# Performance work log

Hardware: AMD Instinct MI355X
Metric: run time of the kernel (lower is better)

Reference implementation:

```python
import jax, jax.numpy as jnp
import numpy as np
from math import sqrt


def setup_inputs() -> dict:
    key = jax.random.key(0)
    k1, k2, k3, k4, k5 = jax.random.split(key, 5)
    B, L, H, D = 16, 4096, 16, 64
    S, M = 4096, 256
    queries = jax.random.normal(k1, (B, L, H, D), dtype=jnp.float32)
    keys = jax.random.normal(k2, (B, S, H, D), dtype=jnp.float32)
    values = jax.random.normal(k3, (B, S, H, D), dtype=jnp.float32)
    # nn.Linear(L_k=S, M): weight [M, S], bias [M]
    squeeze_w = jax.random.normal(k4, (M, S), dtype=jnp.float32) / sqrt(S)
    squeeze_b = jax.random.normal(k5, (M,), dtype=jnp.float32) * 0.01
    return {"queries": queries, "keys": keys, "values": values,
            "squeeze_w": squeeze_w, "squeeze_b": squeeze_b}


def reference(queries, keys, values, squeeze_w, squeeze_b):
    # queries: [B,L,H,D]; keys/values: [B,S,H,D]; squeeze_w: [M,S]; squeeze_b: [M]
    B, L, H, D = queries.shape
    scale = 1.0 / sqrt(D)
    bias = squeeze_b[None, :, None, None]  # broadcast over [B,M,H,D]
    # Linear over the sequence axis S -> M (Linformer compression)
    keys_sq = jnp.einsum('bshd,ms->bmhd', keys, squeeze_w) + bias      # [B,M,H,D]
    values_sq = jnp.einsum('bshd,ms->bmhd', values, squeeze_w) + bias  # [B,M,H,D]
    # Scaled dot-product attention against compressed K/V
    attn = jnp.einsum('blhd,bmhd->bhlm', queries, keys_sq) * scale     # [B,H,L,M]
    attn = jax.nn.softmax(attn, axis=-1)  # dropout is identity in eval / p=0
    context = jnp.einsum('bhlm,bmhd->blhd', attn, values_sq)           # [B,L,H,D]
    return context
```

## Files before the change

kernel.cpp:

```cpp
#include <hip/hip_runtime.h>

#define NB 16
#define NL 4096
#define NH 16
#define ND 64
#define NS 4096
#define NM 256

typedef __fp16 f16;
typedef __attribute__((ext_vector_type(8)))  __fp16 f16x8;
typedef __attribute__((ext_vector_type(4)))  __fp16 f16x4;
typedef __attribute__((ext_vector_type(2)))  __fp16 f16x2;
typedef __attribute__((ext_vector_type(4)))  float  f32x4;
typedef __attribute__((ext_vector_type(16))) float  f32x16;

__device__ __forceinline__ void gload_lds16(const void* g, void* l) {
  __builtin_amdgcn_global_load_lds(
      (const __attribute__((address_space(1))) void*)g,
      (__attribute__((address_space(3))) void*)l, 16, 0, 0);
}

__device__ __forceinline__ int pk2(float a, float b) {
  f16x2 t = __builtin_amdgcn_cvt_pkrtz(a, b);
  union { f16x2 h; int i; } u; u.h = t; return u.i;
}

__global__ __launch_bounds__(256) void k_wcvt(const float* __restrict__ W,
                                              f16* __restrict__ W16) {
  const int i = blockIdx.x * 256 + threadIdx.x;
  f32x4 v = ((const f32x4*)W)[i];
  f16x2 a = __builtin_amdgcn_cvt_pkrtz(v[0], v[1]);
  f16x2 b = __builtin_amdgcn_cvt_pkrtz(v[2], v[3]);
  f16x4 o; o[0] = a[0]; o[1] = a[1]; o[2] = b[0]; o[3] = b[1];
  ((f16x4*)W16)[i] = o;
}

__global__ __launch_bounds__(256, 2) void k_squeeze(
    const f16* __restrict__ W16, const float* __restrict__ keys,
    const float* __restrict__ values, const float* __restrict__ bias,
    f16* __restrict__ Ksq, f16* __restrict__ Vsq) {
  const int h = blockIdx.x & 15;
  const int b = (blockIdx.x >> 4) & 15;
  const int t = blockIdx.x >> 8;
  const float* __restrict__ X = t ? values : keys;

  __shared__ __align__(16) f16 Wt[256 * 64];
  __shared__ __align__(16) f16 XT[64 * 72];

  const int tid  = threadIdx.x;
  const int lane = tid & 63;
  const int w    = tid >> 6;
  const int l31  = lane & 31;
  const int g    = lane >> 5;

  const int  wrsub = lane >> 3;
  const int  wslot = lane & 7;
  const char* Wg = (const char*)W16 + (long)wrsub * (NS * 2) + ((wslot * 16) ^ (wrsub << 4));

  const int sp  = tid & 31;
  const int ng0 = tid >> 5;
  const float* Xb = X + ((long)b * NS) * (NH * ND) + h * ND;

  f32x16 acc[2][2];
#pragma unroll
  for (int mi = 0; mi < 2; ++mi)
#pragma unroll
    for (int di = 0; di < 2; ++di)
#pragma unroll
      for (int q = 0; q < 16; ++q) acc[mi][di][q] = 0.f;

  f32x4 xr[2][2];
#pragma unroll
  for (int u = 0; u < 2; ++u)
#pragma unroll
    for (int r = 0; r < 2; ++r)
      xr[u][r] = *(const f32x4*)(Xb + (long)(2 * sp + r) * (NH * ND) + (ng0 + 8 * u) * 4);

  for (int kt = 0; kt < NS / 64; ++kt) {
    const int k0 = kt * 64;
    __syncthreads();
    {
      const char* wg = Wg + (long)k0 * 2;
#pragma unroll
      for (int i = 0; i < 8; ++i) {
        const int ii = w * 8 + i;
        gload_lds16(wg + (long)ii * 8 * (NS * 2), (char*)Wt + ii * 1024);
      }
    }
#pragma unroll
    for (int u = 0; u < 2; ++u) {
      const int ng = ng0 + 8 * u;
#pragma unroll
      for (int c = 0; c < 4; ++c) {
        f16x2 p = __builtin_amdgcn_cvt_pkrtz(xr[u][0][c], xr[u][1][c]);
        *(f16x2*)((char*)XT + (ng * 4 + c) * 144 + sp * 4) = p;
      }
    }
    __syncthreads();
    if (kt + 1 < NS / 64) {
#pragma unroll
      for (int u = 0; u < 2; ++u)
#pragma unroll
        for (int r = 0; r < 2; ++r)
          xr[u][r] = *(const f32x4*)(Xb + (long)(k0 + 64 + 2 * sp + r) * (NH * ND) +
                                     (ng0 + 8 * u) * 4);
    }
#pragma unroll
    for (int ks = 0; ks < 4; ++ks) {
      f16x8 af[2], bf[2];
#pragma unroll
      for (int mi = 0; mi < 2; ++mi) {
        const int row  = w * 64 + mi * 32 + l31;
        const int colb = (ks * 32 + g * 16) ^ ((row & 7) << 4);
        af[mi] = *(const f16x8*)((const char*)Wt + row * 128 + colb);
      }
#pragma unroll
      for (int di = 0; di < 2; ++di) {
        const int n = di * 32 + l31;
        bf[di] = *(const f16x8*)((const char*)XT + n * 144 + ks * 32 + g * 16);
      }
#pragma unroll
      for (int mi = 0; mi < 2; ++mi)
#pragma unroll
        for (int di = 0; di < 2; ++di)
          acc[mi][di] =
              __builtin_amdgcn_mfma_f32_32x32x16_f16(af[mi], bf[di], acc[mi][di], 0, 0, 0);
    }
  }

  const long bh = b * 16 + h;
  if (t == 0) {
    f16* K = Ksq + bh * (NM * ND);
#pragma unroll
    for (int mi = 0; mi < 2; ++mi)
#pragma unroll
      for (int di = 0; di < 2; ++di)
#pragma unroll
        for (int r = 0; r < 16; ++r) {
          const int m = w * 64 + mi * 32 + (r & 3) + 8 * (r >> 2) + 4 * g;
          const int d = di * 32 + l31;
          K[((d >> 3) * 256 + m) * 8 + (d & 7)] = (f16)(acc[mi][di][r] + bias[m]);
        }
  } else {
    f16* V = Vsq + bh * (ND * NM);
#pragma unroll
    for (int mi = 0; mi < 2; ++mi)
#pragma unroll
      for (int di = 0; di < 2; ++di)
#pragma unroll
        for (int q = 0; q < 4; ++q) {
          const int m0 = w * 64 + mi * 32 + 8 * q + 4 * g;
          const int d  = di * 32 + l31;
          f16x2 p0 = __builtin_amdgcn_cvt_pkrtz(acc[mi][di][q * 4 + 0] + bias[m0 + 0],
                                                acc[mi][di][q * 4 + 1] + bias[m0 + 1]);
          f16x2 p1 = __builtin_amdgcn_cvt_pkrtz(acc[mi][di][q * 4 + 2] + bias[m0 + 2],
                                                acc[mi][di][q * 4 + 3] + bias[m0 + 3]);
          f16x4 pv; pv[0] = p0[0]; pv[1] = p0[1]; pv[2] = p1[0]; pv[3] = p1[1];
          *(f16x4*)(V + ((m0 >> 3) * 64 + d) * 8 + 4 * g) = pv;
        }
  }
}

__global__ __launch_bounds__(256, 2) void k_attn(const float* __restrict__ Q,
                                                 const f16* __restrict__ Ksq,
                                                 const f16* __restrict__ Vsq,
                                                 float* __restrict__ Out) {
  const int xcd   = blockIdx.x & 7;
  const int local = blockIdx.x >> 3;
  const int bh    = xcd * 32 + (local >> 1);
  const int chunk = local & 1;
  const int b = bh >> 4, h = bh & 15;

  __shared__ __align__(16) f16 Klds[8 * 256 * 8];
  __shared__ __align__(16) f16 Vlds[32 * 64 * 8];

  const int tid = threadIdx.x, lane = tid & 63, w = tid >> 6;
  const int q = lane & 31, hi = lane >> 5;

  const float* Qlane = Q   + (((long)b * NL + q) * NH + h) * ND;
  float*       Olane = Out + (((long)b * NL + q) * NH + h) * ND;
  const float  c = 0.125f * 1.44269504088896f;

  f32x4 qv[8];
  {
    const float* qp = Qlane + (long)(chunk * 2048 + w * 32) * (NH * ND) + hi * 8;
#pragma unroll
    for (int kt = 0; kt < 4; ++kt) {
      qv[2 * kt]     = *(const f32x4*)(qp + kt * 16);
      qv[2 * kt + 1] = *(const f32x4*)(qp + kt * 16 + 4);
    }
  }

  {
    const f16* Kg = Ksq + (long)bh * 16384;
    const f16* Vg = Vsq + (long)bh * 16384;
#pragma unroll
    for (int i = 0; i < 8; ++i)
      gload_lds16(Kg + w * 4096 + i * 512 + lane * 8, (char*)Klds + w * 8192 + i * 1024);
#pragma unroll
    for (int i = 0; i < 8; ++i)
      gload_lds16(Vg + w * 4096 + i * 512 + lane * 8, (char*)Vlds + w * 8192 + i * 1024);
  }
  __syncthreads();

  for (int it = 0; it < 16; ++it) {
    const int row0 = chunk * 2048 + it * 128 + w * 32;

    union { f16x8 v; f16x2 h2[4]; } qb[4];
#pragma unroll
    for (int kt = 0; kt < 4; ++kt) {
      qb[kt].h2[0] = __builtin_amdgcn_cvt_pkrtz(qv[2 * kt][0], qv[2 * kt][1]);
      qb[kt].h2[1] = __builtin_amdgcn_cvt_pkrtz(qv[2 * kt][2], qv[2 * kt][3]);
      qb[kt].h2[2] = __builtin_amdgcn_cvt_pkrtz(qv[2 * kt + 1][0], qv[2 * kt + 1][1]);
      qb[kt].h2[3] = __builtin_amdgcn_cvt_pkrtz(qv[2 * kt + 1][2], qv[2 * kt + 1][3]);
    }

    if (it + 1 < 16) {
      const float* qp = Qlane + (long)(row0 + 128) * (NH * ND) + hi * 8;
#pragma unroll
      for (int kt = 0; kt < 4; ++kt) {
        qv[2 * kt]     = *(const f32x4*)(qp + kt * 16);
        qv[2 * kt + 1] = *(const f32x4*)(qp + kt * 16 + 4);
      }
    }

    f32x16 sa[8];
#pragma unroll
    for (int mf = 0; mf < 8; ++mf)
#pragma unroll
      for (int r = 0; r < 16; ++r) sa[mf][r] = 0.f;

#pragma unroll
    for (int kt = 0; kt < 4; ++kt) {
#pragma unroll
      for (int mf = 0; mf < 8; ++mf) {
        f16x8 ka = *(const f16x8*)((const char*)Klds +
                                   ((2 * kt + hi) * 256 + mf * 32 + q) * 16);
        sa[mf] = __builtin_amdgcn_mfma_f32_32x32x16_f16(ka, qb[kt].v, sa[mf], 0, 0, 0);
      }
    }

    f32x16 mm = sa[0];
#pragma unroll
    for (int mf = 1; mf < 8; ++mf)
#pragma unroll
      for (int r = 0; r < 16; ++r) mm[r] = fmaxf(mm[r], sa[mf][r]);
    float m8_0 = fmaxf(mm[0], mm[8]),  m8_1 = fmaxf(mm[1], mm[9]);
    float m8_2 = fmaxf(mm[2], mm[10]), m8_3 = fmaxf(mm[3], mm[11]);
    float m8_4 = fmaxf(mm[4], mm[12]), m8_5 = fmaxf(mm[5], mm[13]);
    float m8_6 = fmaxf(mm[6], mm[14]), m8_7 = fmaxf(mm[7], mm[15]);
    float mx = fmaxf(fmaxf(fmaxf(m8_0, m8_1), fmaxf(m8_2, m8_3)),
                     fmaxf(fmaxf(m8_4, m8_5), fmaxf(m8_6, m8_7)));
    mx = fmaxf(mx, __shfl_xor(mx, 32));

#pragma unroll
    for (int mf = 0; mf < 8; ++mf)
#pragma unroll
      for (int r = 0; r < 16; ++r)
        sa[mf][r] = __builtin_amdgcn_exp2f((sa[mf][r] - mx) * c);

    f32x16 t0 = sa[0] + sa[1];
    f32x16 t1 = sa[2] + sa[3];
    f32x16 t2 = sa[4] + sa[5];
    f32x16 t3 = sa[6] + sa[7];
    t0 = (t0 + t1) + (t2 + t3);
    float s8_0 = t0[0] + t0[8],  s8_1 = t0[1] + t0[9];
    float s8_2 = t0[2] + t0[10], s8_3 = t0[3] + t0[11];
    float s8_4 = t0[4] + t0[12], s8_5 = t0[5] + t0[13];
    float s8_6 = t0[6] + t0[14], s8_7 = t0[7] + t0[15];
    float sum = ((s8_0 + s8_1) + (s8_2 + s8_3)) + ((s8_4 + s8_5) + (s8_6 + s8_7));
    sum += __shfl_xor(sum, 32);
    const float inv = 1.0f / sum;

    f32x16 o[2];
#pragma unroll
    for (int df = 0; df < 2; ++df)
#pragma unroll
      for (int r = 0; r < 16; ++r) o[df][r] = 0.f;

#pragma unroll
    for (int t = 0; t < 16; ++t) {
      const int fp = t >> 1, s = t & 1;
      int a0 = pk2(sa[fp][8 * s + 0] * inv, sa[fp][8 * s + 1] * inv);
      int a1 = pk2(sa[fp][8 * s + 2] * inv, sa[fp][8 * s + 3] * inv);
      int b0 = pk2(sa[fp][8 * s + 4] * inv, sa[fp][8 * s + 5] * inv);
      int b1 = pk2(sa[fp][8 * s + 6] * inv, sa[fp][8 * s + 7] * inv);
      asm volatile("v_permlane32_swap_b32 %0, %1" : "+v"(a0), "+v"(b0));
      asm volatile("v_permlane32_swap_b32 %0, %1" : "+v"(a1), "+v"(b1));
      union { int w4[4]; f16x8 v; } pb;
      pb.w4[0] = a0; pb.w4[1] = a1; pb.w4[2] = b0; pb.w4[3] = b1;
#pragma unroll
      for (int df = 0; df < 2; ++df) {
        f16x8 va = *(const f16x8*)((const char*)Vlds +
                                   ((2 * t + hi) * 64 + df * 32 + q) * 16);
        o[df] = __builtin_amdgcn_mfma_f32_32x32x16_f16(va, pb.v, o[df], 0, 0, 0);
      }
    }

    float* op = Olane + (long)row0 * (NH * ND);
#pragma unroll
    for (int df = 0; df < 2; ++df)
#pragma unroll
      for (int rq = 0; rq < 4; ++rq) {
        f32x4 st;
        st[0] = o[df][rq * 4 + 0]; st[1] = o[df][rq * 4 + 1];
        st[2] = o[df][rq * 4 + 2]; st[3] = o[df][rq * 4 + 3];
        *(f32x4*)(op + df * 32 + rq * 8 + hi * 4) = st;
      }
  }
}

extern "C" void kernel_launch(void* const* d_in, const int* in_sizes, int n_in,
                              void* d_out, int out_size, void* d_ws, size_t ws_size,
                              hipStream_t stream) {
  const float* Qp   = (const float*)d_in[0];
  const float* Kp   = (const float*)d_in[1];
  const float* Vp   = (const float*)d_in[2];
  const float* Wp   = (const float*)d_in[3];
  const float* bp   = (const float*)d_in[4];
  float*       Outp = (float*)d_out;

  char* ws = (char*)d_ws;
  f16* W16 = (f16*)ws;
  f16* Ksq = (f16*)(ws + (2l << 20));
  f16* Vsq = (f16*)(ws + (2l << 20) + (8l << 20));

  hipLaunchKernelGGL(k_wcvt, dim3(1024), dim3(256), 0, stream, Wp, W16);
  hipLaunchKernelGGL(k_squeeze, dim3(512), dim3(256), 0, stream, W16, Kp, Vp, bp, Ksq, Vsq);
  hipLaunchKernelGGL(k_attn, dim3(512), dim3(256), 0, stream, Qp, Ksq, Vsq, Outp);
}
```

Baseline: 315.0 us.

## Pre-swizzle squeeze weights into MFMA layout and read them directly from global

```diff
diff --git a/kernel.cpp b/kernel.cpp
--- a/kernel.cpp
+++ b/kernel.cpp
@@ -26,17 +26,23 @@
 }
 
 __global__ __launch_bounds__(256) void k_wcvt(const float* __restrict__ W,
-                                              f16* __restrict__ W16) {
-  const int i = blockIdx.x * 256 + threadIdx.x;
-  f32x4 v = ((const f32x4*)W)[i];
-  f16x2 a = __builtin_amdgcn_cvt_pkrtz(v[0], v[1]);
-  f16x2 b = __builtin_amdgcn_cvt_pkrtz(v[2], v[3]);
-  f16x4 o; o[0] = a[0]; o[1] = a[1]; o[2] = b[0]; o[3] = b[1];
-  ((f16x4*)W16)[i] = o;
-}
-
-__global__ __launch_bounds__(256, 2) void k_squeeze(
-    const f16* __restrict__ W16, const float* __restrict__ keys,
+                                              f16* __restrict__ Wk) {
+  const int o  = blockIdx.x * 256 + threadIdx.x;
+  const int m  = o & 255;
+  const int kb = o >> 8;
+  const float* src = W + (long)m * NS + kb * 8;
+  f32x4 v0 = *(const f32x4*)(src);
+  f32x4 v1 = *(const f32x4*)(src + 4);
+  union { f16x8 v; f16x2 h2[4]; } pk;
+  pk.h2[0] = __builtin_amdgcn_cvt_pkrtz(v0[0], v0[1]);
+  pk.h2[1] = __builtin_amdgcn_cvt_pkrtz(v0[2], v0[3]);
+  pk.h2[2] = __builtin_amdgcn_cvt_pkrtz(v1[0], v1[1]);
+  pk.h2[3] = __builtin_amdgcn_cvt_pkrtz(v1[2], v1[3]);
+  *(f16x8*)(Wk + (long)o * 8) = pk.v;
+}
+
+__global__ __launch_bounds__(512, 4) void k_squeeze(
+    const f16* __restrict__ Wk, const float* __restrict__ keys,
     const float* __restrict__ values, const float* __restrict__ bias,
     f16* __restrict__ Ksq, f16* __restrict__ Vsq) {
   const int h = blockIdx.x & 15;
@@ -44,8 +50,8 @@
   const int t = blockIdx.x >> 8;
   const float* __restrict__ X = t ? values : keys;
 
-  __shared__ __align__(16) f16 Wt[256 * 64];
-  __shared__ __align__(16) f16 XT[64 * 72];
+  __shared__ __align__(16) f16 XT0[64 * 72];
+  __shared__ __align__(16) f16 XT1[64 * 72];
 
   const int tid  = threadIdx.x;
   const int lane = tid & 63;
@@ -53,78 +59,40 @@
   const int l31  = lane & 31;
   const int g    = lane >> 5;
 
-  const int  wrsub = lane >> 3;
-  const int  wslot = lane & 7;
-  const char* Wg = (const char*)W16 + (long)wrsub * (NS * 2) + ((wslot * 16) ^ (wrsub << 4));
-
-  const int sp  = tid & 31;
-  const int ng0 = tid >> 5;
+  const int sp = tid & 31;
+  const int ng = tid >> 5;
   const float* Xb = X + ((long)b * NS) * (NH * ND) + h * ND;
 
-  f32x16 acc[2][2];
-#pragma unroll
-  for (int mi = 0; mi < 2; ++mi)
-#pragma unroll
-    for (int di = 0; di < 2; ++di)
-#pragma unroll
-      for (int q = 0; q < 16; ++q) acc[mi][di][q] = 0.f;
-
-  f32x4 xr[2][2];
-#pragma unroll
-  for (int u = 0; u < 2; ++u)
-#pragma unroll
-    for (int r = 0; r < 2; ++r)
-      xr[u][r] = *(const f32x4*)(Xb + (long)(2 * sp + r) * (NH * ND) + (ng0 + 8 * u) * 4);
-
-  for (int kt = 0; kt < NS / 64; ++kt) {
-    const int k0 = kt * 64;
+  f32x16 acc[2];
+#pragma unroll
+  for (int di = 0; di < 2; ++di)
+#pragma unroll
+    for (int r = 0; r < 16; ++r) acc[di][r] = 0.f;
+
+  f32x4 xr[2];
+#pragma unroll
+  for (int r = 0; r < 2; ++r)
+    xr[r] = *(const f32x4*)(Xb + (long)(2 * sp + r) * (NH * ND) + ng * 4);
+
+  for (int kt = 0; kt < 64; ++kt) {
+    f16* xt = (kt & 1) ? XT1 : XT0;
+#pragma unroll
+    for (int cc = 0; cc < 4; ++cc)
+      *(int*)((char*)xt + (ng * 4 + cc) * 144 + sp * 4) = pk2(xr[0][cc], xr[1][cc]);
     __syncthreads();
-    {
-      const char* wg = Wg + (long)k0 * 2;
-#pragma unroll
-      for (int i = 0; i < 8; ++i) {
-        const int ii = w * 8 + i;
-        gload_lds16(wg + (long)ii * 8 * (NS * 2), (char*)Wt + ii * 1024);
-      }
-    }
-#pragma unroll
-    for (int u = 0; u < 2; ++u) {
-      const int ng = ng0 + 8 * u;
-#pragma unroll
-      for (int c = 0; c < 4; ++c) {
-        f16x2 p = __builtin_amdgcn_cvt_pkrtz(xr[u][0][c], xr[u][1][c]);
-        *(f16x2*)((char*)XT + (ng * 4 + c) * 144 + sp * 4) = p;
-      }
-    }
-    __syncthreads();
-    if (kt + 1 < NS / 64) {
-#pragma unroll
-      for (int u = 0; u < 2; ++u)
-#pragma unroll
-        for (int r = 0; r < 2; ++r)
-          xr[u][r] = *(const f32x4*)(Xb + (long)(k0 + 64 + 2 * sp + r) * (NH * ND) +
-                                     (ng0 + 8 * u) * 4);
+    if (kt < 63) {
+#pragma unroll
+      for (int r = 0; r < 2; ++r)
+        xr[r] = *(const f32x4*)(Xb + (long)((kt + 1) * 64 + 2 * sp + r) * (NH * ND) + ng * 4);
     }
 #pragma unroll
     for (int ks = 0; ks < 4; ++ks) {
-      f16x8 af[2], bf[2];
-#pragma unroll
-      for (int mi = 0; mi < 2; ++mi) {
-        const int row  = w * 64 + mi * 32 + l31;
-        const int colb = (ks * 32 + g * 16) ^ ((row & 7) << 4);
-        af[mi] = *(const f16x8*)((const char*)Wt + row * 128 + colb);
-      }
-#pragma unroll
-      for (int di = 0; di < 2; ++di) {
-        const int n = di * 32 + l31;
-        bf[di] = *(const f16x8*)((const char*)XT + n * 144 + ks * 32 + g * 16);
-      }
-#pragma unroll
-      for (int mi = 0; mi < 2; ++mi)
-#pragma unroll
-        for (int di = 0; di < 2; ++di)
-          acc[mi][di] =
-              __builtin_amdgcn_mfma_f32_32x32x16_f16(af[mi], bf[di], acc[mi][di], 0, 0, 0);
+      const int kb = kt * 8 + ks * 2 + g;
+      f16x8 af  = *(const f16x8*)(Wk + ((long)kb * 256 + w * 32 + l31) * 8);
+      f16x8 bf0 = *(const f16x8*)((const char*)xt + l31 * 144 + ks * 32 + g * 16);
+      f16x8 bf1 = *(const f16x8*)((const char*)xt + (32 + l31) * 144 + ks * 32 + g * 16);
+      acc[0] = __builtin_amdgcn_mfma_f32_32x32x16_f16(af, bf0, acc[0], 0, 0, 0);
+      acc[1] = __builtin_amdgcn_mfma_f32_32x32x16_f16(af, bf1, acc[1], 0, 0, 0);
     }
   }
 
@@ -132,32 +100,28 @@
   if (t == 0) {
     f16* K = Ksq + bh * (NM * ND);
 #pragma unroll
-    for (int mi = 0; mi < 2; ++mi)
-#pragma unroll
-      for (int di = 0; di < 2; ++di)
-#pragma unroll
-        for (int r = 0; r < 16; ++r) {
-          const int m = w * 64 + mi * 32 + (r & 3) + 8 * (r >> 2) + 4 * g;
-          const int d = di * 32 + l31;
-          K[((d >> 3) * 256 + m) * 8 + (d & 7)] = (f16)(acc[mi][di][r] + bias[m]);
-        }
+    for (int di = 0; di < 2; ++di)
+#pragma unroll
+      for (int r = 0; r < 16; ++r) {
+        const int m = w * 32 + (r & 3) + 8 * (r >> 2) + 4 * g;
+        const int d = di * 32 + l31;
+        K[((d >> 3) * 256 + m) * 8 + (d & 7)] = (f16)(acc[di][r] + bias[m]);
+      }
   } else {
     f16* V = Vsq + bh * (ND * NM);
 #pragma unroll
-    for (int mi = 0; mi < 2; ++mi)
-#pragma unroll
-      for (int di = 0; di < 2; ++di)
-#pragma unroll
-        for (int q = 0; q < 4; ++q) {
-          const int m0 = w * 64 + mi * 32 + 8 * q + 4 * g;
-          const int d  = di * 32 + l31;
-          f16x2 p0 = __builtin_amdgcn_cvt_pkrtz(acc[mi][di][q * 4 + 0] + bias[m0 + 0],
-                                                acc[mi][di][q * 4 + 1] + bias[m0 + 1]);
-          f16x2 p1 = __builtin_amdgcn_cvt_pkrtz(acc[mi][di][q * 4 + 2] + bias[m0 + 2],
-                                                acc[mi][di][q * 4 + 3] + bias[m0 + 3]);
-          f16x4 pv; pv[0] = p0[0]; pv[1] = p0[1]; pv[2] = p1[0]; pv[3] = p1[1];
-          *(f16x4*)(V + ((m0 >> 3) * 64 + d) * 8 + 4 * g) = pv;
-        }
+    for (int di = 0; di < 2; ++di)
+#pragma unroll
+      for (int qq = 0; qq < 4; ++qq) {
+        const int m0 = w * 32 + 8 * qq + 4 * g;
+        const int d  = di * 32 + l31;
+        f16x2 p0 = __builtin_amdgcn_cvt_pkrtz(acc[di][qq * 4 + 0] + bias[m0 + 0],
+                                              acc[di][qq * 4 + 1] + bias[m0 + 1]);
+        f16x2 p1 = __builtin_amdgcn_cvt_pkrtz(acc[di][qq * 4 + 2] + bias[m0 + 2],
+                                              acc[di][qq * 4 + 3] + bias[m0 + 3]);
+        f16x4 pv; pv[0] = p0[0]; pv[1] = p0[1]; pv[2] = p1[0]; pv[3] = p1[1];
+        *(f16x4*)(V + ((m0 >> 3) * 64 + d) * 8 + 4 * g) = pv;
+      }
   }
 }
 
@@ -321,11 +285,11 @@
   float*       Outp = (float*)d_out;
 
   char* ws = (char*)d_ws;
-  f16* W16 = (f16*)ws;
+  f16* Wk  = (f16*)ws;
   f16* Ksq = (f16*)(ws + (2l << 20));
   f16* Vsq = (f16*)(ws + (2l << 20) + (8l << 20));
 
-  hipLaunchKernelGGL(k_wcvt, dim3(1024), dim3(256), 0, stream, Wp, W16);
-  hipLaunchKernelGGL(k_squeeze, dim3(512), dim3(256), 0, stream, W16, Kp, Vp, bp, Ksq, Vsq);
+  hipLaunchKernelGGL(k_wcvt, dim3(512), dim3(256), 0, stream, Wp, Wk);
+  hipLaunchKernelGGL(k_squeeze, dim3(512), dim3(512), 0, stream, Wk, Kp, Vp, bp, Ksq, Vsq);
   hipLaunchKernelGGL(k_attn, dim3(512), dim3(256), 0, stream, Qp, Ksq, Vsq, Outp);
 }
```

New measurement: 334.9 us. 1.06x slower.
